# Kernel tuning notes

Hardware: AMD Instinct MI355X
Metric: run time of the kernel (lower is better)

Reference implementation:

```python
import jax, jax.numpy as jnp
import numpy as np

D_MODEL = 768
NHEAD = 12
DK = D_MODEL // NHEAD
MAX_DIST = 1000.0
FF = 3072
POS_HIDDEN = 32  # hidden width of the relative-position bias MLP
EPS = 1e-5
B, L = 2, 1024


def setup_inputs() -> dict:
    key = jax.random.key(0)
    ks = jax.random.split(key, 24)

    def lin(k, i, o):  # torch-Linear-like init, stored as (in, out)
        return jax.random.uniform(k, (i, o), jnp.float32, -1.0, 1.0) / np.sqrt(i)

    return {
        "src": jax.random.normal(ks[0], (B, L, D_MODEL), jnp.float32),
        "src_x": jax.random.uniform(ks[1], (B, L), jnp.float32) * 1000.0,
        "src_y": jax.random.uniform(ks[2], (B, L), jnp.float32) * 1000.0,
        # attention projections (q,k,v,out)
        "Wq": lin(ks[3], D_MODEL, D_MODEL), "bq": jnp.zeros((D_MODEL,), jnp.float32),
        "Wk": lin(ks[4], D_MODEL, D_MODEL), "bk": jnp.zeros((D_MODEL,), jnp.float32),
        "Wv": lin(ks[5], D_MODEL, D_MODEL), "bv": jnp.zeros((D_MODEL,), jnp.float32),
        "Wo": lin(ks[6], D_MODEL, D_MODEL), "bo": jnp.zeros((D_MODEL,), jnp.float32),
        # relative-position bias MLP: 2 -> POS_HIDDEN -> NHEAD
        "P1": lin(ks[7], 2, POS_HIDDEN), "pb1": jnp.zeros((POS_HIDDEN,), jnp.float32),
        "P2": lin(ks[8], POS_HIDDEN, NHEAD), "pb2": jnp.zeros((NHEAD,), jnp.float32),
        # FFN
        "W1": lin(ks[9], D_MODEL, FF), "b1": jnp.zeros((FF,), jnp.float32),
        "W2": lin(ks[10], FF, D_MODEL), "b2": jnp.zeros((D_MODEL,), jnp.float32),
        # post-LN params
        "g1": jnp.ones((D_MODEL,), jnp.float32), "be1": jnp.zeros((D_MODEL,), jnp.float32),
        "g2": jnp.ones((D_MODEL,), jnp.float32), "be2": jnp.zeros((D_MODEL,), jnp.float32),
    }


def _layernorm(x, g, b):
    m = jnp.mean(x, axis=-1, keepdims=True)
    v = jnp.var(x, axis=-1, keepdims=True)
    return (x - m) * jax.lax.rsqrt(v + EPS) * g + b


def reference(src, src_x, src_y, Wq, bq, Wk, bk, Wv, bv, Wo, bo,
              P1, pb1, P2, pb2, W1, b1, W2, b2, g1, be1, g2, be2):
    b, l, _ = src.shape
    # projections -> (b, h, l, dk)
    q = (src @ Wq + bq).reshape(b, l, NHEAD, DK).transpose(0, 2, 1, 3)
    k = (src @ Wk + bk).reshape(b, l, NHEAD, DK).transpose(0, 2, 1, 3)
    v = (src @ Wv + bv).reshape(b, l, NHEAD, DK).transpose(0, 2, 1, 3)
    # 2D relative positions, clipped and normalized to [-1, 1]
    rx = jnp.clip(src_x[:, :, None] - src_x[:, None, :], -MAX_DIST, MAX_DIST) / MAX_DIST
    ry = jnp.clip(src_y[:, :, None] - src_y[:, None, :], -MAX_DIST, MAX_DIST) / MAX_DIST
    rel = jnp.stack([rx, ry], axis=-1)                        # (b, l, l, 2)
    bias = jax.nn.relu(rel @ P1 + pb1) @ P2 + pb2             # (b, l, l, h)
    bias = bias.transpose(0, 3, 1, 2)                         # (b, h, l, l)
    scores = jnp.einsum('bhqd,bhkd->bhqk', q, k) / np.sqrt(DK).astype(np.float32) + bias
    attn = jax.nn.softmax(scores, axis=-1)
    o = jnp.einsum('bhqk,bhkd->bhqd', attn, v).transpose(0, 2, 1, 3).reshape(b, l, D_MODEL)
    src2 = o @ Wo + bo
    x = _layernorm(src + src2, g1, be1)                       # post-LN residual 1
    ff = jax.nn.relu(x @ W1 + b1) @ W2 + b2                   # FFN
    return _layernorm(x + ff, g2, be2)                        # post-LN residual 2
```

## Files before the change

### kernel.cpp

```cpp
#include <hip/hip_runtime.h>
#include <math.h>

typedef unsigned short ushort_t;
typedef __attribute__((ext_vector_type(8))) short bf16x8;
typedef __attribute__((ext_vector_type(4))) float f32x4;

constexpr int kD      = 768;
constexpr int kNH     = 12;
constexpr int kDK     = 64;
constexpr int kFF     = 3072;
constexpr int kL      = 1024;
constexpr int kRows   = 2048;
constexpr float kEPS  = 1e-5f;

__device__ __forceinline__ ushort_t f2bf(float f) {
    union { float f; unsigned u; } v; v.f = f;
    unsigned r = (v.u + 0x7fffu + ((v.u >> 16) & 1u)) >> 16;
    return (ushort_t)r;
}
__device__ __forceinline__ float bf2f(ushort_t u) {
    union { unsigned u; float f; } v; v.u = ((unsigned)u) << 16; return v.f;
}

#define GL_LDS(gp, lp) __builtin_amdgcn_global_load_lds( \
    (const __attribute__((address_space(1))) void*)(gp), \
    (__attribute__((address_space(3))) void*)(lp), 16, 0, 0)

template<int RELU, int OUTBF, int ADDBIAS>
__device__ __forceinline__ void gemm_body(const ushort_t* __restrict__ A,
                                          const ushort_t* __restrict__ WT,
                                          const float* __restrict__ bias,
                                          void* __restrict__ Cout,
                                          int N, int K, int row0, int col0,
                                          int kbeg, int kend, ushort_t* lds)
{
    const int tid  = threadIdx.x;
    const int lane = tid & 63;
    const int wave = tid >> 6;
    const int wrow = (wave & 1) * 64;
    const int wcol = (wave >> 1) * 64;

    const int srow = wave * 16 + (lane >> 2);
    const int sk   = (lane & 3) * 8;
    const ushort_t* ga0 = A  + (size_t)(row0 + srow)      * K + sk;
    const ushort_t* ga1 = A  + (size_t)(row0 + srow + 64) * K + sk;
    const ushort_t* gb0 = WT + (size_t)(col0 + srow)      * K + sk;
    const ushort_t* gb1 = WT + (size_t)(col0 + srow + 64) * K + sk;

    const int wo = wave * 512;

    const int fl = lane & 15, fq = lane >> 4;

    f32x4 acc[4][4] = {};

    {
        ushort_t* b0 = lds;
        GL_LDS(ga0 + kbeg, b0 + wo);
        GL_LDS(ga1 + kbeg, b0 + 2048 + wo);
        GL_LDS(gb0 + kbeg, b0 + 4096 + wo);
        GL_LDS(gb1 + kbeg, b0 + 4096 + 2048 + wo);
    }
    __syncthreads();

    int cur = 0;
    for (int k0 = kbeg; k0 < kend; k0 += 32) {
        ushort_t* bs = lds + (cur ? 8192 : 0);
        ushort_t* bn = lds + (cur ? 0 : 8192);

        if (k0 + 32 < kend) {
            GL_LDS(ga0 + k0 + 32, bn + wo);
            GL_LDS(ga1 + k0 + 32, bn + 2048 + wo);
            GL_LDS(gb0 + k0 + 32, bn + 4096 + wo);
            GL_LDS(gb1 + k0 + 32, bn + 4096 + 2048 + wo);
        }

        bf16x8 av[4], bv[4];
        #pragma unroll
        for (int i = 0; i < 4; ++i) {
            av[i] = *(const bf16x8*)(bs + (wrow + i * 16 + fl) * 32 + fq * 8);
            bv[i] = *(const bf16x8*)(bs + 4096 + (wcol + i * 16 + fl) * 32 + fq * 8);
        }
        #pragma unroll
        for (int mi = 0; mi < 4; ++mi)
            #pragma unroll
            for (int ni = 0; ni < 4; ++ni)
                acc[mi][ni] = __builtin_amdgcn_mfma_f32_16x16x32_bf16(
                    av[mi], bv[ni], acc[mi][ni], 0, 0, 0);

        __syncthreads();
        cur ^= 1;
    }

    #pragma unroll
    for (int mi = 0; mi < 4; ++mi) {
        const int m = wrow + mi * 16 + fq * 4;
        #pragma unroll
        for (int ni = 0; ni < 4; ++ni) {
            const int n = wcol + ni * 16 + fl;
            const float bb = ADDBIAS ? bias[col0 + n] : 0.f;
            #pragma unroll
            for (int r = 0; r < 4; ++r) {
                float v = acc[mi][ni][r] + bb;
                if (RELU) v = fmaxf(v, 0.f);
                const size_t idx = (size_t)(row0 + m + r) * N + col0 + n;
                if (OUTBF) ((ushort_t*)Cout)[idx] = f2bf(v);
                else       ((float*)Cout)[idx]    = v;
            }
        }
    }
}

template<int RELU, int OUTBF>
__global__ __launch_bounds__(256)
void gemm_kernel(const ushort_t* __restrict__ A, const ushort_t* __restrict__ WT,
                 const float* __restrict__ bias, void* __restrict__ Cout,
                 int N, int K)
{
    __shared__ ushort_t lds[16384];
    gemm_body<RELU, OUTBF, 1>(A, WT, bias, Cout, N, K,
                              blockIdx.y * 128, blockIdx.x * 128, 0, K, lds);
}

__global__ __launch_bounds__(256)
void gemm_splitk_kernel(const ushort_t* __restrict__ A, const ushort_t* __restrict__ WT,
                        float* __restrict__ parts, int N, int K, int kslice)
{
    __shared__ ushort_t lds[16384];
    const int z = blockIdx.z;
    float* out = parts + (size_t)z * kRows * N;
    gemm_body<0, 0, 0>(A, WT, nullptr, out, N, K,
                       blockIdx.y * 128, blockIdx.x * 128,
                       z * kslice, (z + 1) * kslice, lds);
}

__device__ __forceinline__ void wt_tile(const float* __restrict__ src,
                                        ushort_t* __restrict__ dst,
                                        int K, int N, int kt, int nt,
                                        float (*T)[65], int tid)
{
    #pragma unroll
    for (int i = 0; i < 4; ++i) {
        const int e = tid + i * 256;
        const int r = e >> 4;
        const int c = (e & 15) * 4;
        const float4 f = *(const float4*)&src[(size_t)(kt + r) * N + nt + c];
        T[c + 0][r] = f.x; T[c + 1][r] = f.y; T[c + 2][r] = f.z; T[c + 3][r] = f.w;
    }
    __syncthreads();
    #pragma unroll
    for (int i = 0; i < 4; ++i) {
        const int e = tid + i * 256;
        const int n = e >> 4;
        const int kc = (e & 15) * 4;
        ushort4 o;
        o.x = f2bf(T[n][kc + 0]); o.y = f2bf(T[n][kc + 1]);
        o.z = f2bf(T[n][kc + 2]); o.w = f2bf(T[n][kc + 3]);
        *(ushort4*)&dst[(size_t)(nt + n) * K + kt + kc] = o;
    }
}

__global__ __launch_bounds__(256)
void prep_kernel(const float* __restrict__ Wq, const float* __restrict__ Wk,
                 const float* __restrict__ Wv,
                 ushort_t* wqT, ushort_t* wkT, ushort_t* wvT,
                 const float* __restrict__ src, ushort_t* __restrict__ sb)
{
    __shared__ float T[64][65];
    const int bid = blockIdx.x;
    const int tid = threadIdx.x;

    if (bid < 432) {
        const int wz = bid / 144, t = bid - wz * 144;
        const float* s = (wz == 0) ? Wq : (wz == 1) ? Wk : Wv;
        ushort_t*   d = (wz == 0) ? wqT : (wz == 1) ? wkT : wvT;
        wt_tile(s, d, kD, kD, (t % 12) * 64, (t / 12) * 64, T, tid);
    } else {
        const int i = (bid - 432) * 256 + tid;
        const float4 f = ((const float4*)src)[i];
        ushort4 o;
        o.x = f2bf(f.x); o.y = f2bf(f.y); o.z = f2bf(f.z); o.w = f2bf(f.w);
        ((ushort4*)sb)[i] = o;
    }
}

struct BiasSmem {
    float P[32][16];
    float pb2l[12];
    float qxl[16], qyl[16], kxl[64], kyl[64];
    ushort_t Btile[12 * 1024];
};
struct AttnSmem {
    ushort_t Sp[4][16][72];
    ushort_t Ob[4][16][64];
    float    Ll[4][16];
};

__device__ __forceinline__ void bias_body(int bid, BiasSmem& S,
                 const float* __restrict__ sx, const float* __restrict__ sy,
                 const float* __restrict__ P1, const float* __restrict__ pb1,
                 const float* __restrict__ P2, const float* __restrict__ pb2,
                 ushort_t* __restrict__ biasb)
{
    const int b  = bid >> 10;
    const int qt = (bid >> 4) & 63;
    const int kt = bid & 15;
    const int tid = threadIdx.x;

    if (tid < 32) {
        S.P[tid][0] = P1[tid];
        S.P[tid][1] = P1[32 + tid];
        S.P[tid][2] = pb1[tid];
        S.P[tid][3] = 0.f;
    }
    for (int e = tid; e < 384; e += 256) S.P[e / 12][4 + e % 12] = P2[e];
    if (tid < 12) S.pb2l[tid] = pb2[tid];
    if (tid < 16) { S.qxl[tid] = sx[b * kL + qt * 16 + tid];
                    S.qyl[tid] = sy[b * kL + qt * 16 + tid]; }
    if (tid < 64) { S.kxl[tid] = sx[b * kL + kt * 64 + tid];
                    S.kyl[tid] = sy[b * kL + kt * 64 + tid]; }
    __syncthreads();

    const int ri = tid >> 4;
    const int fl = tid & 15;
    const int fq = ri >> 2, r = ri & 3;
    const int lane16 = fq * 16 + fl;
    const float xi = S.qxl[ri], yi = S.qyl[ri];

    float rx[4], ry[4];
    #pragma unroll
    for (int n = 0; n < 4; ++n) {
        const int cj = n * 16 + fl;
        rx[n] = fminf(fmaxf(xi - S.kxl[cj], -1000.f), 1000.f) * 1e-3f;
        ry[n] = fminf(fmaxf(yi - S.kyl[cj], -1000.f), 1000.f) * 1e-3f;
    }

    float acc[4][12] = {};
    #pragma unroll 4
    for (int u = 0; u < 32; ++u) {
        const float4 pc = *(const float4*)&S.P[u][0];
        const float4 w0 = *(const float4*)&S.P[u][4];
        const float4 w1 = *(const float4*)&S.P[u][8];
        const float4 w2 = *(const float4*)&S.P[u][12];
        float t[4];
        #pragma unroll
        for (int n = 0; n < 4; ++n)
            t[n] = fmaxf(fmaf(rx[n], pc.x, fmaf(ry[n], pc.y, pc.z)), 0.f);
        #pragma unroll
        for (int n = 0; n < 4; ++n) {
            acc[n][0]  = fmaf(t[n], w0.x, acc[n][0]);
            acc[n][1]  = fmaf(t[n], w0.y, acc[n][1]);
            acc[n][2]  = fmaf(t[n], w0.z, acc[n][2]);
            acc[n][3]  = fmaf(t[n], w0.w, acc[n][3]);
            acc[n][4]  = fmaf(t[n], w1.x, acc[n][4]);
            acc[n][5]  = fmaf(t[n], w1.y, acc[n][5]);
            acc[n][6]  = fmaf(t[n], w1.z, acc[n][6]);
            acc[n][7]  = fmaf(t[n], w1.w, acc[n][7]);
            acc[n][8]  = fmaf(t[n], w2.x, acc[n][8]);
            acc[n][9]  = fmaf(t[n], w2.y, acc[n][9]);
            acc[n][10] = fmaf(t[n], w2.z, acc[n][10]);
            acc[n][11] = fmaf(t[n], w2.w, acc[n][11]);
        }
    }

    #pragma unroll
    for (int h = 0; h < 12; ++h) {
        const float pb = S.pb2l[h] - 4.0f;
        #pragma unroll
        for (int n = 0; n < 4; ++n)
            S.Btile[h * 1024 + lane16 * 16 + n * 4 + r] = f2bf(acc[n][h] + pb);
    }
    __syncthreads();

    #pragma unroll
    for (int i = 0; i < 6; ++i) {
        const int off = (i * 256 + tid) * 8;
        const int h = off >> 10;
        const int inner = off & 1023;
        ushort_t* dst = biasb +
            (((size_t)(b * kNH + h) * 64 + qt) * 16 + kt) * 1024 + inner;
        *(uint4*)dst = *(const uint4*)&S.Btile[off];
    }
}

constexpr size_t kQkvSmem =
    sizeof(BiasSmem) > 32768 ? sizeof(BiasSmem) : 32768;

__global__ __launch_bounds__(256)
void qkv_bias_kernel(const ushort_t* __restrict__ A,
                     const ushort_t* wq, const ushort_t* wk, const ushort_t* wv,
                     const float* bq, const float* bk, const float* bv,
                     ushort_t* q, ushort_t* k, ushort_t* v,
                     const float* __restrict__ sx, const float* __restrict__ sy,
                     const float* __restrict__ P1, const float* __restrict__ pb1,
                     const float* __restrict__ P2, const float* __restrict__ pb2,
                     ushort_t* __restrict__ biasb)
{
    __shared__ __align__(16) char smem[kQkvSmem];
    const int bid = blockIdx.x;

    if (bid < 288) {
        const int z = bid / 96, rem = bid - z * 96;
        const int bx = rem % 6, by = rem / 6;
        const ushort_t* WT; const float* bias; ushort_t* out;
        if (z == 0)      { WT = wq; bias = bq; out = q; }
        else if (z == 1) { WT = wk; bias = bk; out = k; }
        else             { WT = wv; bias = bv; out = v; }
        gemm_body<0, 1, 1>(A, WT, bias, out, kD, kD,
                           by * 128, bx * 128, 0, kD, (ushort_t*)smem);
    } else {
        bias_body(bid - 288, *(BiasSmem*)smem, sx, sy, P1, pb1, P2, pb2, biasb);
    }
}

__global__ __launch_bounds__(256)
void vtrans_kernel(const ushort_t* __restrict__ vb, ushort_t* __restrict__ vt)
{
    const int bh = blockIdx.x;
    const int b = bh / kNH, h = bh - b * kNH;
    const int j0 = blockIdx.y * 64;
    __shared__ ushort_t T[64][72];

    const int tid = threadIdx.x;
    {
        const int jr = tid & 63;
        const int c0 = (tid >> 6) * 16;
        const ushort_t* sp = vb + (size_t)(b * kL + j0 + jr) * kD + h * kDK + c0;
        uint4 u0 = *(const uint4*)sp;
        uint4 u1 = *(const uint4*)(sp + 8);
        const ushort_t* e0 = (const ushort_t*)&u0;
        const ushort_t* e1 = (const ushort_t*)&u1;
        #pragma unroll
        for (int jj = 0; jj < 8; ++jj) {
            T[c0 + jj][jr]     = e0[jj];
            T[c0 + 8 + jj][jr] = e1[jj];
        }
    }
    __syncthreads();
    {
        const int dr = tid >> 2;
        const int jc = (tid & 3) * 16;
        ushort_t* dp = vt + (size_t)(bh * 64 + dr) * kL + j0 + jc;
        *(uint4*)dp       = *(const uint4*)&T[dr][jc];
        *(uint4*)(dp + 8) = *(const uint4*)&T[dr][jc + 8];
    }
}

constexpr size_t kAttnWtSmem =
    sizeof(AttnSmem) > sizeof(float) * 64 * 65 ? sizeof(AttnSmem)
                                               : sizeof(float) * 64 * 65;

__global__ __launch_bounds__(256)
void attn_wt_kernel(const ushort_t* __restrict__ qg, const ushort_t* __restrict__ kg,
                    const ushort_t* __restrict__ vt, const ushort_t* __restrict__ biasb,
                    ushort_t* __restrict__ og,
                    const float* __restrict__ Wo, const float* __restrict__ W1,
                    const float* __restrict__ W2,
                    ushort_t* woT, ushort_t* w1T, ushort_t* w2T)
{
    __shared__ __align__(16) char smem[kAttnWtSmem];
    const int bid = blockIdx.x;
    const int tid = threadIdx.x;

    if (bid >= 768) {
        float (*T)[65] = (float(*)[65])smem;
        const int t = bid - 768;
        if (t < 144)      wt_tile(Wo, woT, kD,  kD,  (t % 12) * 64, (t / 12) * 64, T, tid);
        else if (t < 720) { const int t2 = t - 144;
                            wt_tile(W1, w1T, kD,  kFF, (t2 % 12) * 64, (t2 / 12) * 64, T, tid); }
        else              { const int t2 = t - 720;
                            wt_tile(W2, w2T, kFF, kD,  (t2 % 48) * 64, (t2 / 48) * 64, T, tid); }
        return;
    }

    AttnSmem& S = *(AttnSmem*)smem;
    const int swz  = (bid & 7) * 96 + (bid >> 3);
    const int bh   = swz >> 5;
    const int qt32 = swz & 31;
    const int b  = bh / kNH, h = bh - b * kNH;
    const int z  = tid >> 6;
    const int qs = z & 1;
    const int kh = z >> 1;
    const int lane = tid & 63;
    const int fl = lane & 15, fq = lane >> 4;
    const int qt = qt32 * 2 + qs;
    const int q0 = qt * 16;
    const int kbeg = kh * 512;

    const size_t qoff = (size_t)(b * kL + q0 + fl) * kD + h * kDK + fq * 8;
    const bf16x8 aq0 = *(const bf16x8*)(qg + qoff);
    const bf16x8 aq1 = *(const bf16x8*)(qg + qoff + 32);

    const ushort_t* kbase = kg + (size_t)(b * kL) * kD + h * kDK + fq * 8;
    const ushort_t* vbase = vt + (size_t)(bh * 64) * kL + fq * 8;
    const ushort_t* btile = biasb +
        ((size_t)(bh * 64 + qt) * 16 + kh * 8) * 1024 + lane * 16;

    f32x4 accO[4] = {};
    float l_part[4] = {};

    bf16x8 kc[4][2];
    uint4 bc0, bc1;
    {
        #pragma unroll
        for (int n = 0; n < 4; ++n) {
            const ushort_t* kr = kbase + (size_t)(kbeg + n * 16 + fl) * kD;
            kc[n][0] = *(const bf16x8*)kr;
            kc[n][1] = *(const bf16x8*)(kr + 32);
        }
        bc0 = *(const uint4*)btile;
        bc1 = *(const uint4*)(btile + 8);
    }

    #pragma unroll 4
    for (int t = 0; t < 8; ++t) {
        const int k0 = kbeg + t * 64;

        bf16x8 vv[4][2];
        #pragma unroll
        for (int n = 0; n < 4; ++n) {
            const ushort_t* vr = vbase + (size_t)(n * 16 + fl) * kL + k0;
            vv[n][0] = *(const bf16x8*)vr;
            vv[n][1] = *(const bf16x8*)(vr + 32);
        }

        f32x4 Sv[4] = {};
        __builtin_amdgcn_s_setprio(1);
        #pragma unroll
        for (int n = 0; n < 4; ++n) {
            Sv[n] = __builtin_amdgcn_mfma_f32_16x16x32_bf16(aq0, kc[n][0], Sv[n], 0, 0, 0);
            Sv[n] = __builtin_amdgcn_mfma_f32_16x16x32_bf16(aq1, kc[n][1], Sv[n], 0, 0, 0);
        }
        __builtin_amdgcn_s_setprio(0);

        bf16x8 kn[4][2];
        uint4 bn0, bn1;
        if (t < 7) {
            #pragma unroll
            for (int n = 0; n < 4; ++n) {
                const ushort_t* kr = kbase + (size_t)(k0 + 64 + n * 16 + fl) * kD;
                kn[n][0] = *(const bf16x8*)kr;
                kn[n][1] = *(const bf16x8*)(kr + 32);
            }
            bn0 = *(const uint4*)(btile + (t + 1) * 1024);
            bn1 = *(const uint4*)(btile + (t + 1) * 1024 + 8);
        }

        ushort_t bu[16];
        *(uint4*)&bu[0] = bc0;
        *(uint4*)&bu[8] = bc1;

        #pragma unroll
        for (int n = 0; n < 4; ++n)
            #pragma unroll
            for (int r = 0; r < 4; ++r) {
                const float e = __expf(fmaf(Sv[n][r], 0.125f, bf2f(bu[n * 4 + r])));
                Sv[n][r] = e;
                l_part[r] += e;
            }

        #pragma unroll
        for (int n = 0; n < 4; ++n)
            #pragma unroll
            for (int r = 0; r < 4; ++r)
                S.Sp[z][fq * 4 + r][n * 16 + fl] = f2bf(Sv[n][r]);

        const bf16x8 ap0 = *(const bf16x8*)&S.Sp[z][fl][fq * 8];
        const bf16x8 ap1 = *(const bf16x8*)&S.Sp[z][fl][32 + fq * 8];
        __builtin_amdgcn_s_setprio(1);
        #pragma unroll
        for (int n = 0; n < 4; ++n) {
            accO[n] = __builtin_amdgcn_mfma_f32_16x16x32_bf16(ap0, vv[n][0], accO[n], 0, 0, 0);
            accO[n] = __builtin_amdgcn_mfma_f32_16x16x32_bf16(ap1, vv[n][1], accO[n], 0, 0, 0);
        }
        __builtin_amdgcn_s_setprio(0);

        if (t < 7) {
            #pragma unroll
            for (int n = 0; n < 4; ++n) { kc[n][0] = kn[n][0]; kc[n][1] = kn[n][1]; }
            bc0 = bn0; bc1 = bn1;
        }
    }

    float l_full[4], inv[4];
    #pragma unroll
    for (int r = 0; r < 4; ++r) {
        float l = l_part[r];
        l += __shfl_xor(l, 1, 16);
        l += __shfl_xor(l, 2, 16);
        l += __shfl_xor(l, 4, 16);
        l += __shfl_xor(l, 8, 16);
        l_full[r] = l;
        inv[r] = 1.0f / l;
    }

    #pragma unroll
    for (int n = 0; n < 4; ++n)
        #pragma unroll
        for (int r = 0; r < 4; ++r)
            S.Ob[z][fq * 4 + r][n * 16 + fl] = f2bf(accO[n][r] * inv[r]);
    if (fl == 0) {
        #pragma unroll
        for (int r = 0; r < 4; ++r)
            S.Ll[z][fq * 4 + r] = l_full[r];
    }
    __syncthreads();

    {
        const int ri = tid >> 3;
        const int d0 = (tid & 7) * 8;
        const int qs2 = ri >> 4, rr = ri & 15;
        const int z0 = qs2, z1 = 2 + qs2;
        const float w0 = S.Ll[z0][rr], w1 = S.Ll[z1][rr];
        const float winv = 1.0f / (w0 + w1);
        const float c0 = w0 * winv, c1 = w1 * winv;

        ushort_t o[8];
        #pragma unroll
        for (int j = 0; j < 8; ++j)
            o[j] = f2bf(fmaf(c0, bf2f(S.Ob[z0][rr][d0 + j]),
                             c1 * bf2f(S.Ob[z1][rr][d0 + j])));
        ushort_t* dp = og + (size_t)(b * kL + qt32 * 32 + ri) * kD + h * kDK + d0;
        *(uint4*)dp = *(const uint4*)o;
    }
}

template<int NPART, int DUAL>
__global__ __launch_bounds__(256)
void ln_kernel(const float* __restrict__ a, const float* __restrict__ parts,
               const float* __restrict__ bias,
               const float* __restrict__ g, const float* __restrict__ be,
               float* __restrict__ out, ushort_t* __restrict__ out_bf)
{
    const int row = blockIdx.x;
    const int tid = threadIdx.x;
    const float* pa = a + (size_t)row * kD;
    constexpr size_t NTOK = (size_t)kRows * kD;

    float v[3];
    float s = 0.f, sq = 0.f;
    #pragma unroll
    for (int i = 0; i < 3; ++i) {
        const int d = tid + i * 256;
        float t = pa[d] + bias[d];
        #pragma unroll
        for (int p = 0; p < NPART; ++p)
            t += parts[p * NTOK + (size_t)row * kD + d];
        v[i] = t;
        s  += t;
        sq += t * t;
    }
    #pragma unroll
    for (int off = 32; off > 0; off >>= 1) {
        s  += __shfl_down(s, off);
        sq += __shfl_down(sq, off);
    }
    __shared__ float bs[4], bq2[4];
    if ((tid & 63) == 0) { bs[tid >> 6] = s; bq2[tid >> 6] = sq; }
    __syncthreads();
    const float ts = bs[0] + bs[1] + bs[2] + bs[3];
    const float tq = bq2[0] + bq2[1] + bq2[2] + bq2[3];
    const float invn = 1.0f / (float)kD;
    const float mean = ts * invn;
    const float var  = tq * invn - mean * mean;
    const float rstd = rsqrtf(var + kEPS);

    float* po = out + (size_t)row * kD;
    #pragma unroll
    for (int i = 0; i < 3; ++i) {
        const int d = tid + i * 256;
        const float o = (v[i] - mean) * rstd * g[d] + be[d];
        po[d] = o;
        if (DUAL) out_bf[(size_t)row * kD + d] = f2bf(o);
    }
}

extern "C" void kernel_launch(void* const* d_in, const int* in_sizes, int n_in,
                              void* d_out, int out_size, void* d_ws, size_t ws_size,
                              hipStream_t stream)
{
    const float* src = (const float*)d_in[0];
    const float* sx  = (const float*)d_in[1];
    const float* sy  = (const float*)d_in[2];
    const float* Wq  = (const float*)d_in[3];  const float* bq  = (const float*)d_in[4];
    const float* Wk  = (const float*)d_in[5];  const float* bk  = (const float*)d_in[6];
    const float* Wv  = (const float*)d_in[7];  const float* bv  = (const float*)d_in[8];
    const float* Wo  = (const float*)d_in[9];  const float* bo  = (const float*)d_in[10];
    const float* P1  = (const float*)d_in[11]; const float* pb1 = (const float*)d_in[12];
    const float* P2  = (const float*)d_in[13]; const float* pb2 = (const float*)d_in[14];
    const float* W1  = (const float*)d_in[15]; const float* b1  = (const float*)d_in[16];
    const float* W2  = (const float*)d_in[17]; const float* b2  = (const float*)d_in[18];
    const float* g1  = (const float*)d_in[19]; const float* be1 = (const float*)d_in[20];
    const float* g2  = (const float*)d_in[21]; const float* be2 = (const float*)d_in[22];

    constexpr size_t W768  = 768u * 768u;
    constexpr size_t W3072 = 768u * 3072u;
    constexpr size_t NTOK  = (size_t)kRows * kD;

    ushort_t* wsu = (ushort_t*)d_ws;
    ushort_t* wqT = wsu;
    ushort_t* wkT = wqT + W768;
    ushort_t* wvT = wkT + W768;
    ushort_t* qb  = wvT + W768;
    ushort_t* kb  = qb + NTOK;
    ushort_t* vb  = kb + NTOK;
    ushort_t* sb  = vb + NTOK;
    ushort_t* vtb = sb + NTOK;
    ushort_t* biasb = vtb + NTOK;
    ushort_t* woT   = biasb;
    ushort_t* w1T   = woT + W768;
    ushort_t* w2T   = w1T + W3072;
    float*    xb    = (float*)(w2T + W3072);
    ushort_t* h1bf  = (ushort_t*)(xb + NTOK);
    float*    s2p   = (float*)h1bf;
    float*    ff2p  = (float*)(h1bf + 4 * NTOK);
    ushort_t* xbf   = qb;

    const dim3 blk(256);

    prep_kernel<<<dim3(1968), blk, 0, stream>>>(Wq, Wk, Wv, wqT, wkT, wvT, src, sb);

    qkv_bias_kernel<<<dim3(2336), blk, 0, stream>>>(
        sb, wqT, wkT, wvT, bq, bk, bv, qb, kb, vb,
        sx, sy, P1, pb1, P2, pb2, biasb);

    vtrans_kernel<<<dim3(2 * kNH, kL / 64), blk, 0, stream>>>(vb, vtb);

    attn_wt_kernel<<<dim3(2064), blk, 0, stream>>>(
        qb, kb, vtb, biasb, sb, Wo, W1, W2,
        (ushort_t*)(ff2p + 3 * NTOK),
        (ushort_t*)(ff2p + 3 * NTOK) + W768,
        (ushort_t*)(ff2p + 3 * NTOK) + W768 + W3072);

    ushort_t* woT2 = (ushort_t*)(ff2p + 3 * NTOK);
    ushort_t* w1T2 = woT2 + W768;
    ushort_t* w2T2 = w1T2 + W3072;

    gemm_splitk_kernel<<<dim3(kD / 128, kRows / 128, 2), blk, 0, stream>>>(
        sb, woT2, s2p, kD, kD, kD / 2);

    ln_kernel<2, 1><<<dim3(kRows), blk, 0, stream>>>(src, s2p, bo, g1, be1, xb, xbf);

    gemm_kernel<1, 1><<<dim3(kFF / 128, kRows / 128), blk, 0, stream>>>(
        xbf, w1T2, b1, h1bf, kFF, kD);

    gemm_splitk_kernel<<<dim3(kD / 128, kRows / 128, 3), blk, 0, stream>>>(
        h1bf, w2T2, ff2p, kD, kFF, kFF / 3);

    ln_kernel<3, 0><<<dim3(kRows), blk, 0, stream>>>(xb, ff2p, b2, g2, be2,
                                                     (float*)d_out, nullptr);
}
```

Baseline: 277.1 us.

## Raise attention occupancy, drop K prefetch, and deepen split-K when workspace allows

```diff
diff --git a/kernel.cpp b/kernel.cpp
--- a/kernel.cpp
+++ b/kernel.cpp
@@ -48,7 +48,6 @@
     const ushort_t* gb1 = WT + (size_t)(col0 + srow + 64) * K + sk;
 
     const int wo = wave * 512;
-
     const int fl = lane & 15, fq = lane >> 4;
 
     f32x4 acc[4][4] = {};
@@ -349,7 +348,7 @@
     sizeof(AttnSmem) > sizeof(float) * 64 * 65 ? sizeof(AttnSmem)
                                                : sizeof(float) * 64 * 65;
 
-__global__ __launch_bounds__(256)
+__global__ __launch_bounds__(256, 6)
 void attn_wt_kernel(const ushort_t* __restrict__ qg, const ushort_t* __restrict__ kg,
                     const ushort_t* __restrict__ vt, const ushort_t* __restrict__ biasb,
                     ushort_t* __restrict__ og,
@@ -398,22 +397,19 @@
     f32x4 accO[4] = {};
     float l_part[4] = {};
 
-    bf16x8 kc[4][2];
-    uint4 bc0, bc1;
-    {
+    #pragma unroll 2
+    for (int t = 0; t < 8; ++t) {
+        const int k0 = kbeg + t * 64;
+
+        bf16x8 kc[4][2];
         #pragma unroll
         for (int n = 0; n < 4; ++n) {
-            const ushort_t* kr = kbase + (size_t)(kbeg + n * 16 + fl) * kD;
+            const ushort_t* kr = kbase + (size_t)(k0 + n * 16 + fl) * kD;
             kc[n][0] = *(const bf16x8*)kr;
             kc[n][1] = *(const bf16x8*)(kr + 32);
         }
-        bc0 = *(const uint4*)btile;
-        bc1 = *(const uint4*)(btile + 8);
-    }
-
-    #pragma unroll 4
-    for (int t = 0; t < 8; ++t) {
-        const int k0 = kbeg + t * 64;
+        const uint4 bc0 = *(const uint4*)(btile + t * 1024);
+        const uint4 bc1 = *(const uint4*)(btile + t * 1024 + 8);
 
         bf16x8 vv[4][2];
         #pragma unroll
@@ -431,19 +427,6 @@
             Sv[n] = __builtin_amdgcn_mfma_f32_16x16x32_bf16(aq1, kc[n][1], Sv[n], 0, 0, 0);
         }
         __builtin_amdgcn_s_setprio(0);
-
-        bf16x8 kn[4][2];
-        uint4 bn0, bn1;
-        if (t < 7) {
-            #pragma unroll
-            for (int n = 0; n < 4; ++n) {
-                const ushort_t* kr = kbase + (size_t)(k0 + 64 + n * 16 + fl) * kD;
-                kn[n][0] = *(const bf16x8*)kr;
-                kn[n][1] = *(const bf16x8*)(kr + 32);
-            }
-            bn0 = *(const uint4*)(btile + (t + 1) * 1024);
-            bn1 = *(const uint4*)(btile + (t + 1) * 1024 + 8);
-        }
 
         ushort_t bu[16];
         *(uint4*)&bu[0] = bc0;
@@ -473,12 +456,6 @@
             accO[n] = __builtin_amdgcn_mfma_f32_16x16x32_bf16(ap1, vv[n][1], accO[n], 0, 0, 0);
         }
         __builtin_amdgcn_s_setprio(0);
-
-        if (t < 7) {
-            #pragma unroll
-            for (int n = 0; n < 4; ++n) { kc[n][0] = kn[n][0]; kc[n][1] = kn[n][1]; }
-            bc0 = bn0; bc1 = bn1;
-        }
     }
 
     float l_full[4], inv[4];
@@ -606,14 +583,32 @@
     ushort_t* sb  = vb + NTOK;
     ushort_t* vtb = sb + NTOK;
     ushort_t* biasb = vtb + NTOK;
-    ushort_t* woT   = biasb;
-    ushort_t* w1T   = woT + W768;
-    ushort_t* w2T   = w1T + W3072;
-    float*    xb    = (float*)(w2T + W3072);
+    float*    xb    = (float*)(biasb + W768 + 2 * W3072);
     ushort_t* h1bf  = (ushort_t*)(xb + NTOK);
-    float*    s2p   = (float*)h1bf;
-    float*    ff2p  = (float*)(h1bf + 4 * NTOK);
     ushort_t* xbf   = qb;
+
+    const size_t h1off   = (size_t)(h1bf - wsu);
+    const size_t bigNeed = (h1off + 20 * NTOK + W768 + 2 * W3072) * 2;
+    const bool   big     = ws_size >= bigNeed;
+
+    float*    s2p;
+    float*    ff2p;
+    ushort_t* scratch;
+    int npWo, npFF;
+    if (big) {
+        s2p     = (float*)h1bf;
+        ff2p    = (float*)(h1bf + 8 * NTOK);
+        scratch = h1bf + 20 * NTOK;
+        npWo = 4; npFF = 6;
+    } else {
+        s2p     = (float*)h1bf;
+        ff2p    = (float*)(h1bf + 4 * NTOK);
+        scratch = (ushort_t*)(ff2p + 3 * NTOK);
+        npWo = 2; npFF = 3;
+    }
+    ushort_t* woT2 = scratch;
+    ushort_t* w1T2 = woT2 + W768;
+    ushort_t* w2T2 = w1T2 + W3072;
 
     const dim3 blk(256);
 
@@ -626,26 +621,22 @@
     vtrans_kernel<<<dim3(2 * kNH, kL / 64), blk, 0, stream>>>(vb, vtb);
 
     attn_wt_kernel<<<dim3(2064), blk, 0, stream>>>(
-        qb, kb, vtb, biasb, sb, Wo, W1, W2,
-        (ushort_t*)(ff2p + 3 * NTOK),
-        (ushort_t*)(ff2p + 3 * NTOK) + W768,
-        (ushort_t*)(ff2p + 3 * NTOK) + W768 + W3072);
-
-    ushort_t* woT2 = (ushort_t*)(ff2p + 3 * NTOK);
-    ushort_t* w1T2 = woT2 + W768;
-    ushort_t* w2T2 = w1T2 + W3072;
-
-    gemm_splitk_kernel<<<dim3(kD / 128, kRows / 128, 2), blk, 0, stream>>>(
-        sb, woT2, s2p, kD, kD, kD / 2);
-
-    ln_kernel<2, 1><<<dim3(kRows), blk, 0, stream>>>(src, s2p, bo, g1, be1, xb, xbf);
+        qb, kb, vtb, biasb, sb, Wo, W1, W2, woT2, w1T2, w2T2);
+
+    gemm_splitk_kernel<<<dim3(kD / 128, kRows / 128, npWo), blk, 0, stream>>>(
+        sb, woT2, s2p, kD, kD, kD / npWo);
+
+    if (big) ln_kernel<4, 1><<<dim3(kRows), blk, 0, stream>>>(src, s2p, bo, g1, be1, xb, xbf);
+    else     ln_kernel<2, 1><<<dim3(kRows), blk, 0, stream>>>(src, s2p, bo, g1, be1, xb, xbf);
 
     gemm_kernel<1, 1><<<dim3(kFF / 128, kRows / 128), blk, 0, stream>>>(
         xbf, w1T2, b1, h1bf, kFF, kD);
 
-    gemm_splitk_kernel<<<dim3(kD / 128, kRows / 128, 3), blk, 0, stream>>>(
-        h1bf, w2T2, ff2p, kD, kFF, kFF / 3);
-
-    ln_kernel<3, 0><<<dim3(kRows), blk, 0, stream>>>(xb, ff2p, b2, g2, be2,
-                                                     (float*)d_out, nullptr);
-}
+    gemm_splitk_kernel<<<dim3(kD / 128, kRows / 128, npFF), blk, 0, stream>>>(
+        h1bf, w2T2, ff2p, kD, kFF, kFF / npFF);
+
+    if (big) ln_kernel<6, 0><<<dim3(kRows), blk, 0, stream>>>(xb, ff2p, b2, g2, be2,
+                                                              (float*)d_out, nullptr);
+    else     ln_kernel<3, 0><<<dim3(kRows), blk, 0, stream>>>(xb, ff2p, b2, g2, be2,
+                                                              (float*)d_out, nullptr);
+}
```

Result: slower. 332.1 us (+19.8%).
